# Performance work log

Hardware: AMD Instinct MI355X
Metric: run time of the kernel (lower is better)

## Reference

```python
import jax, jax.numpy as jnp
import numpy as np

DECAY = 0.6
THRESH = 0.6
MASK_T = 784 * 4  # default T in create_general_mask


def _make_mask(dim, c_min=10, c_max=50, min_dc=0.95, max_dc=0.99, T=MASK_T):
    # Faithful numpy port of create_general_mask (phase_shift_max=0.0 -> no shift).
    dcs = np.linspace(min_dc, max_dc, dim)
    cycles = np.linspace(c_min, c_max, dim)
    rows = []
    for cyc, dc in zip(cycles, dcs):
        cyc = int(np.ceil(cyc))
        on = int(np.ceil(dc * cyc))
        pat = [1] * on + [0] * (cyc - on)
        full = pat * (T // cyc) + pat[: T % cyc]
        rows.append(full)
    return jnp.asarray(np.array(rows, dtype=np.float32))  # [dim, T]


def setup_inputs() -> dict:
    key = jax.random.key(0)
    k1, k2, k3, k4, k5 = jax.random.split(key, 5)
    T, B, NTOKEN, NINP, H1, H2 = 128, 32, 32000, 256, 512, 512
    raw_input = jax.random.randint(k1, (T, B), 0, NTOKEN)
    enc_w = jax.random.uniform(k2, (NTOKEN, NINP), jnp.float32, -0.1, 0.1)
    # kaiming_uniform-like init: bound = sqrt(6 / fan_in), torch fan_in = dim 1
    b1 = float(np.sqrt(6.0 / H1))
    b2 = float(np.sqrt(6.0 / H2))
    fc1 = jax.random.uniform(k3, (NINP, H1), jnp.float32, -b1, b1)
    fc2 = jax.random.uniform(k4, (H1, H2), jnp.float32, -b2, b2)
    dec_w = jax.random.uniform(k5, (NTOKEN, H2), jnp.float32, -0.1, 0.1)
    dec_b = jnp.zeros((NTOKEN,), jnp.float32)
    mask1 = _make_mask(H1)
    mask2 = _make_mask(H2)
    return {"raw_input": raw_input, "enc_w": enc_w, "fc1": fc1, "fc2": fc2,
            "dec_w": dec_w, "dec_b": dec_b, "mask1": mask1, "mask2": mask2}


def _act(x):
    # ActFun.forward: heaviside spike
    return (x > 0.0).astype(x.dtype)


def reference(raw_input, enc_w, fc1, fc2, dec_w, dec_b, mask1, mask2):
    T, B = raw_input.shape
    emb = enc_w[raw_input]                    # [T, B, ninp] (dropout p=0 -> identity)
    m1 = mask1[:, :T].T                       # [T, H1]
    m2 = mask2[:, :T].T                       # [T, H2]

    def rhythm_update(fc, x, mem, m):
        state = x @ fc                        # [B, H]
        reset = (mem > THRESH).astype(x.dtype)
        new_mem = mem * (1.0 - reset) * DECAY + state
        mem = jnp.where(m == 0.0, mem, new_mem)   # mask broadcasts [H] -> [B, H]
        spike = _act(mem - THRESH) * m
        return mem, spike

    h1 = jnp.zeros((B, fc1.shape[1]), emb.dtype)
    h2 = jnp.zeros((B, fc2.shape[1]), emb.dtype)

    def step(carry, xs):
        h1m, h2m = carry
        x, ma, mb = xs
        h1m, s1 = rhythm_update(fc1, x, h1m, ma)
        h2m, s2 = rhythm_update(fc2, s1, h2m, mb)
        return (h1m, h2m), s2

    _, spikes = jax.lax.scan(step, (h1, h2), (emb, m1, m2))  # [T, B, H2]
    decoded = spikes @ dec_w.T + dec_b        # [T, B, ntoken]
    return decoded
```

## Files before the change

### kernel.cpp

```cpp
#include <hip/hip_runtime.h>


typedef __attribute__((ext_vector_type(8))) short short8;
typedef __attribute__((ext_vector_type(4))) float f32x4;
typedef __attribute__((ext_vector_type(8))) unsigned short us8;

#define WAITVM(N) asm volatile("s_waitcnt vmcnt(" #N ")" ::: "memory")
#define LGKM0()   asm volatile("s_waitcnt lgkmcnt(0)" ::: "memory")

__device__ __forceinline__ unsigned short f2bf(float f) {
    unsigned int u = __float_as_uint(f);
    unsigned int r = (u + 0x7FFFu + ((u >> 16) & 1u)) >> 16;
    return (unsigned short)r;
}

__global__ __launch_bounds__(256) void maskT_kernel(
    const float* __restrict__ m1, const float* __restrict__ m2,
    float* __restrict__ t1, float* __restrict__ t2)
{
    int i = blockIdx.x * 256 + threadIdx.x;
    int h = i >> 7, t = i & 127;
    t1[t * 512 + h] = m1[(size_t)h * 3136 + t];
    t2[t * 512 + h] = m2[(size_t)h * 3136 + t];
}

__global__ __launch_bounds__(256) void split_kernel(
    const float* __restrict__ w, unsigned short* __restrict__ w2, int n4)
{
    int i = blockIdx.x * 256 + threadIdx.x;
    if (i >= n4) return;
    float4 v = ((const float4*)w)[i];
    float vv[4] = {v.x, v.y, v.z, v.w};
    us8 o;
    #pragma unroll
    for (int c = 0; c < 4; ++c) {
        unsigned short hb = f2bf(vv[c]);
        float hf = __uint_as_float(((unsigned int)hb) << 16);
        o[2 * c]     = hb;
        o[2 * c + 1] = f2bf(vv[c] - hf);
    }
    ((us8*)w2)[i] = o;
}

__global__ __launch_bounds__(256) void gemm_f32_kernel(
    const float* __restrict__ A, const float* __restrict__ B,
    float* __restrict__ C, int M, int N, int K,
    const int* __restrict__ gidx, const float* __restrict__ gtable)
{
    __shared__ float As[16][64];
    __shared__ float Bs[16][64];
    int tid = threadIdx.x;
    int bn0 = blockIdx.x * 64, bm0 = blockIdx.y * 64;

    int lrowA = tid >> 2;
    int lkA   = (tid & 3) * 4;
    int lkB   = tid >> 4;
    int lnB   = (tid & 15) * 4;
    int ty = tid >> 4, tx = tid & 15;

    const float* Abase;
    size_t aoff;
    int grow = bm0 + lrowA;
    if (gidx) { Abase = gtable; aoff = (size_t)gidx[grow] * K; }
    else      { Abase = A;      aoff = (size_t)grow * K; }

    float acc[4][4];
    #pragma unroll
    for (int i = 0; i < 4; ++i)
        #pragma unroll
        for (int j = 0; j < 4; ++j) acc[i][j] = 0.f;

    for (int k0 = 0; k0 < K; k0 += 16) {
        float4 av = *(const float4*)(Abase + aoff + k0 + lkA);
        As[lkA + 0][lrowA] = av.x;
        As[lkA + 1][lrowA] = av.y;
        As[lkA + 2][lrowA] = av.z;
        As[lkA + 3][lrowA] = av.w;
        float4 bv = *(const float4*)(B + (size_t)(k0 + lkB) * N + bn0 + lnB);
        *(float4*)&Bs[lkB][lnB] = bv;
        __syncthreads();
        #pragma unroll
        for (int kk = 0; kk < 16; ++kk) {
            float4 aq = *(float4*)&As[kk][ty * 4];
            float4 bq = *(float4*)&Bs[kk][tx * 4];
            float aa[4] = {aq.x, aq.y, aq.z, aq.w};
            float bb[4] = {bq.x, bq.y, bq.z, bq.w};
            #pragma unroll
            for (int i = 0; i < 4; ++i)
                #pragma unroll
                for (int j = 0; j < 4; ++j) acc[i][j] += aa[i] * bb[j];
        }
        __syncthreads();
    }
    #pragma unroll
    for (int i = 0; i < 4; ++i) {
        float4 v = {acc[i][0], acc[i][1], acc[i][2], acc[i][3]};
        *(float4*)(C + (size_t)(bm0 + ty * 4 + i) * N + bn0 + tx * 4) = v;
    }
}

template <int DUP>
__global__ __launch_bounds__(64) void scan_kernel(
    const float* __restrict__ state, const float* __restrict__ maskT,
    float* __restrict__ outF, unsigned int* __restrict__ outU)
{
    int tid = blockIdx.x * 64 + threadIdx.x;
    int b = tid >> 9, h = tid & 511;
    float mem = 0.f;
    for (int t0 = 0; t0 < 128; t0 += 8) {
        float st8[8], m8[8];
        #pragma unroll
        for (int u = 0; u < 8; ++u) {
            st8[u] = state[(size_t)((t0 + u) * 32 + b) * 512 + h];
            m8[u]  = maskT[(t0 + u) * 512 + h];
        }
        #pragma unroll
        for (int u = 0; u < 8; ++u) {
            float nm = (mem > 0.6f) ? st8[u] : mem * 0.6f + st8[u];
            mem = (m8[u] == 0.0f) ? mem : nm;
            float spf = (mem > 0.6f) ? m8[u] : 0.0f;
            size_t ridx = (size_t)((t0 + u) * 32 + b) * 512 + h;
            if (DUP) outU[ridx] = f2bf(spf) * 0x10001u;
            else     outF[ridx] = spf;
        }
    }
}

__global__ __launch_bounds__(512, 2) void gemm3_kernel(
    const unsigned short* __restrict__ A,
    const unsigned short* __restrict__ W,
    const float* __restrict__ bias, float* __restrict__ C)
{
    constexpr int K = 1024, NTOK = 32000;
    __shared__ char lds[131072];

    int tid  = threadIdx.x;
    int lane = tid & 63;
    int wid  = __builtin_amdgcn_readfirstlane(tid >> 6);

    int bid = blockIdx.x;
    int swz = (bid & 7) * 250 + (bid >> 3);
    int mt = swz & 15;
    int nt = swz >> 4;
    int m0 = mt * 256, n0 = nt * 256;

    int wm = wid >> 2, wn = wid & 3;

    const unsigned short* srcB[4];
    int dstOff[4];
    #pragma unroll
    for (int i = 0; i < 4; ++i) {
        int q   = i * 512 + tid;
        int isB = q >> 10;
        int qq  = q & 1023;
        int j   = qq >> 3;
        int cp  = qq & 7;
        int c   = cp ^ (j & 7);
        int row = 2 * j + (c >> 2);
        srcB[i] = (isB ? W + (size_t)(n0 + row) * K
                       : A + (size_t)(m0 + row) * K) + (c & 3) * 8;
        dstOff[i] = (i * 512 + wid * 64) * 16;
    }

    int r = lane & 15, co = lane >> 4;
    int aOff[8], bOff[4];
    #pragma unroll
    for (int mf = 0; mf < 8; ++mf) {
        int row = wm * 128 + mf * 16 + r;
        int j = row >> 1, c = co + 4 * (row & 1);
        aOff[mf] = (j * 8 + (c ^ (j & 7))) * 16;
    }
    #pragma unroll
    for (int nf = 0; nf < 4; ++nf) {
        int row = wn * 64 + nf * 16 + r;
        int j = row >> 1, c = co + 4 * (row & 1);
        bOff[nf] = 16384 + (j * 8 + (c ^ (j & 7))) * 16;
    }

    f32x4 acc[8][4];
    #pragma unroll
    for (int i = 0; i < 8; ++i)
        #pragma unroll
        for (int j = 0; j < 4; ++j) acc[i][j] = (f32x4){0.f, 0.f, 0.f, 0.f};

    auto GLOAD = [&](int i, int kt) {
        __builtin_amdgcn_global_load_lds(
            (const __attribute__((address_space(1))) unsigned int*)(srcB[i] + kt * 32),
            (__attribute__((address_space(3))) unsigned int*)(lds + ((kt & 3) << 15) + dstOff[i]),
            16, 0, 0);
    };

    auto STEP = [&](int t, bool stage) {
        const char* base = lds + ((t & 3) << 15);
        short8 fa0[4], fb[4], fa1[4];
        if (stage) { GLOAD(0, t + 3); GLOAD(1, t + 3); }
        #pragma unroll
        for (int f = 0; f < 4; ++f) fa0[f] = *(const short8*)(base + aOff[f]);
        #pragma unroll
        for (int f = 0; f < 4; ++f) fb[f]  = *(const short8*)(base + bOff[f]);
        __builtin_amdgcn_s_barrier();
        LGKM0();
        __builtin_amdgcn_s_setprio(1);
        #pragma unroll
        for (int mf = 0; mf < 4; ++mf)
            #pragma unroll
            for (int nf = 0; nf < 4; ++nf)
                acc[mf][nf] = __builtin_amdgcn_mfma_f32_16x16x32_bf16(
                    fa0[mf], fb[nf], acc[mf][nf], 0, 0, 0);
        __builtin_amdgcn_s_setprio(0);
        __builtin_amdgcn_s_barrier();
        if (stage) { GLOAD(2, t + 3); GLOAD(3, t + 3); }
        #pragma unroll
        for (int f = 0; f < 4; ++f) fa1[f] = *(const short8*)(base + aOff[4 + f]);
        __builtin_amdgcn_s_barrier();
        LGKM0();
        __builtin_amdgcn_s_setprio(1);
        #pragma unroll
        for (int mf = 0; mf < 4; ++mf)
            #pragma unroll
            for (int nf = 0; nf < 4; ++nf)
                acc[4 + mf][nf] = __builtin_amdgcn_mfma_f32_16x16x32_bf16(
                    fa1[mf], fb[nf], acc[4 + mf][nf], 0, 0, 0);
        __builtin_amdgcn_s_setprio(0);
    };

    #pragma unroll
    for (int kt = 0; kt < 3; ++kt)
        #pragma unroll
        for (int i = 0; i < 4; ++i) GLOAD(i, kt);
    WAITVM(8);
    __builtin_amdgcn_s_barrier();

    for (int t = 0; t < 29; ++t) {
        STEP(t, true);
        WAITVM(8);
        __builtin_amdgcn_s_barrier();
    }
    STEP(29, false);
    WAITVM(4);
    __builtin_amdgcn_s_barrier();
    STEP(30, false);
    WAITVM(0);
    __builtin_amdgcn_s_barrier();
    STEP(31, false);

    int lr = lane >> 4, lc = lane & 15;
    #pragma unroll
    for (int nf = 0; nf < 4; ++nf) {
        int gc = n0 + wn * 64 + nf * 16 + lc;
        float bv = bias[gc];
        #pragma unroll
        for (int mf = 0; mf < 8; ++mf) {
            int gr = m0 + wm * 128 + mf * 16 + lr * 4;
            f32x4 v = acc[mf][nf];
            #pragma unroll
            for (int j = 0; j < 4; ++j)
                C[(size_t)(gr + j) * NTOK + gc] = v[j] + bv;
        }
    }
}

extern "C" void kernel_launch(void* const* d_in, const int* in_sizes, int n_in,
                              void* d_out, int out_size, void* d_ws, size_t ws_size,
                              hipStream_t stream)
{
    const int*   raw   = (const int*)  d_in[0];
    const float* enc_w = (const float*)d_in[1];
    const float* fc1   = (const float*)d_in[2];
    const float* fc2   = (const float*)d_in[3];
    const float* dec_w = (const float*)d_in[4];
    const float* dec_b = (const float*)d_in[5];
    const float* mask1 = (const float*)d_in[6];
    const float* mask2 = (const float*)d_in[7];
    float* out = (float*)d_out;

    const int H1 = 512, H2 = 512, NINP = 256, NTOK = 32000;
    const int M = 128 * 32;

    char* ws = (char*)d_ws;
    float*          st  = (float*)ws;
    float*          spF = (float*)(ws + (size_t)(8u << 20));
    unsigned int*   a2u = (unsigned int*)(ws + (size_t)(8u << 20));
    unsigned short* A2  = (unsigned short*)(ws + (size_t)(8u << 20));
    unsigned short* W2  = (unsigned short*)(ws + (size_t)(16u << 20));
    float* mT1 = (float*)d_out;
    float* mT2 = (float*)d_out + 65536;

    maskT_kernel<<<256, 256, 0, stream>>>(mask1, mask2, mT1, mT2);

    int n4 = NTOK * H2 / 4;
    split_kernel<<<(n4 + 255) / 256, 256, 0, stream>>>(dec_w, W2, n4);

    gemm_f32_kernel<<<dim3(H1 / 64, M / 64), 256, 0, stream>>>(
        nullptr, fc1, st, M, H1, NINP, raw, enc_w);

    scan_kernel<0><<<256, 64, 0, stream>>>(st, mT1, spF, nullptr);

    gemm_f32_kernel<<<dim3(H2 / 64, M / 64), 256, 0, stream>>>(
        spF, fc2, st, M, H2, H1, nullptr, nullptr);

    scan_kernel<1><<<256, 64, 0, stream>>>(st, mT2, nullptr, a2u);

    gemm3_kernel<<<(M / 256) * (NTOK / 256), 512, 0, stream>>>(A2, W2, dec_b, out);

    (void)in_sizes; (void)n_in; (void)out_size; (void)ws_size;
}
```

Before: 932.5 us.

## Switch decoder GEMM to 32x32x16 MFMA and enlarge fp32 GEMM tiles

The decoder GEMM moves from 16x16x32 bf16 MFMA fragments to 32x32x16 fragments. The LDS fragment offsets, the per-k-half loads and the epilogue row mapping are rewritten to match, so fewer, larger MFMAs and fewer LDS reads are issued per step. Separately, the fp32 GEMMs for fc1 and fc2 now use a 128x64 tile with K=32 per stage, padded LDS, and global loads issued before the barrier, which halves the grid. The cost is more registers per thread in the fp32 GEMM, more complex index mapping, and fewer blocks for small GEMMs.

```diff
diff --git a/kernel.cpp b/kernel.cpp
--- a/kernel.cpp
+++ b/kernel.cpp
@@ -1,9 +1,9 @@
 #include <hip/hip_runtime.h>
 
 
-typedef __attribute__((ext_vector_type(8))) short short8;
-typedef __attribute__((ext_vector_type(4))) float f32x4;
-typedef __attribute__((ext_vector_type(8))) unsigned short us8;
+typedef __attribute__((ext_vector_type(8)))  short short8;
+typedef __attribute__((ext_vector_type(16))) float f32x16;
+typedef __attribute__((ext_vector_type(8)))  unsigned short us8;
 
 #define WAITVM(N) asm volatile("s_waitcnt vmcnt(" #N ")" ::: "memory")
 #define LGKM0()   asm volatile("s_waitcnt lgkmcnt(0)" ::: "memory")
@@ -47,55 +47,70 @@
     float* __restrict__ C, int M, int N, int K,
     const int* __restrict__ gidx, const float* __restrict__ gtable)
 {
-    __shared__ float As[16][64];
-    __shared__ float Bs[16][64];
+    __shared__ float As[32][132];
+    __shared__ float Bs[32][68];
     int tid = threadIdx.x;
-    int bn0 = blockIdx.x * 64, bm0 = blockIdx.y * 64;
-
-    int lrowA = tid >> 2;
-    int lkA   = (tid & 3) * 4;
-    int lkB   = tid >> 4;
-    int lnB   = (tid & 15) * 4;
+    int bn0 = blockIdx.x * 64, bm0 = blockIdx.y * 128;
     int ty = tid >> 4, tx = tid & 15;
 
+    int arL  = tid >> 1;
+    int akh  = (tid & 1) * 16;
     const float* Abase;
     size_t aoff;
-    int grow = bm0 + lrowA;
-    if (gidx) { Abase = gtable; aoff = (size_t)gidx[grow] * K; }
-    else      { Abase = A;      aoff = (size_t)grow * K; }
-
-    float acc[4][4];
-    #pragma unroll
-    for (int i = 0; i < 4; ++i)
+    {
+        int grow = bm0 + arL;
+        if (gidx) { Abase = gtable; aoff = (size_t)gidx[grow] * K; }
+        else      { Abase = A;      aoff = (size_t)grow * K; }
+    }
+
+    float acc[8][4];
+    #pragma unroll
+    for (int i = 0; i < 8; ++i)
         #pragma unroll
         for (int j = 0; j < 4; ++j) acc[i][j] = 0.f;
 
-    for (int k0 = 0; k0 < K; k0 += 16) {
-        float4 av = *(const float4*)(Abase + aoff + k0 + lkA);
-        As[lkA + 0][lrowA] = av.x;
-        As[lkA + 1][lrowA] = av.y;
-        As[lkA + 2][lrowA] = av.z;
-        As[lkA + 3][lrowA] = av.w;
-        float4 bv = *(const float4*)(B + (size_t)(k0 + lkB) * N + bn0 + lnB);
-        *(float4*)&Bs[lkB][lnB] = bv;
+    for (int k0 = 0; k0 < K; k0 += 32) {
+        float4 a4[4];
+        #pragma unroll
+        for (int i = 0; i < 4; ++i)
+            a4[i] = *(const float4*)(Abase + aoff + k0 + akh + i * 4);
+        float4 b4[2];
+        #pragma unroll
+        for (int i = 0; i < 2; ++i) {
+            int f = tid + 256 * i;
+            b4[i] = *(const float4*)(B + (size_t)(k0 + (f >> 4)) * N + bn0 + (f & 15) * 4);
+        }
         __syncthreads();
         #pragma unroll
-        for (int kk = 0; kk < 16; ++kk) {
-            float4 aq = *(float4*)&As[kk][ty * 4];
-            float4 bq = *(float4*)&Bs[kk][tx * 4];
-            float aa[4] = {aq.x, aq.y, aq.z, aq.w};
+        for (int i = 0; i < 4; ++i) {
+            As[akh + i * 4 + 0][arL] = a4[i].x;
+            As[akh + i * 4 + 1][arL] = a4[i].y;
+            As[akh + i * 4 + 2][arL] = a4[i].z;
+            As[akh + i * 4 + 3][arL] = a4[i].w;
+        }
+        #pragma unroll
+        for (int i = 0; i < 2; ++i) {
+            int f = tid + 256 * i;
+            *(float4*)&Bs[f >> 4][(f & 15) * 4] = b4[i];
+        }
+        __syncthreads();
+        #pragma unroll
+        for (int kk = 0; kk < 32; ++kk) {
+            float a8[8];
+            *(float4*)&a8[0] = *(const float4*)&As[kk][ty * 8];
+            *(float4*)&a8[4] = *(const float4*)&As[kk][ty * 8 + 4];
+            float4 bq = *(const float4*)&Bs[kk][tx * 4];
             float bb[4] = {bq.x, bq.y, bq.z, bq.w};
             #pragma unroll
-            for (int i = 0; i < 4; ++i)
+            for (int i = 0; i < 8; ++i)
                 #pragma unroll
-                for (int j = 0; j < 4; ++j) acc[i][j] += aa[i] * bb[j];
-        }
-        __syncthreads();
-    }
-    #pragma unroll
-    for (int i = 0; i < 4; ++i) {
+                for (int j = 0; j < 4; ++j) acc[i][j] += a8[i] * bb[j];
+        }
+    }
+    #pragma unroll
+    for (int i = 0; i < 8; ++i) {
         float4 v = {acc[i][0], acc[i][1], acc[i][2], acc[i][3]};
-        *(float4*)(C + (size_t)(bm0 + ty * 4 + i) * N + bn0 + tx * 4) = v;
+        *(float4*)(C + (size_t)(bm0 + ty * 8 + i) * N + bn0 + tx * 4) = v;
     }
 }
 
@@ -162,26 +177,30 @@
         dstOff[i] = (i * 512 + wid * 64) * 16;
     }
 
-    int r = lane & 15, co = lane >> 4;
-    int aOff[8], bOff[4];
-    #pragma unroll
-    for (int mf = 0; mf < 8; ++mf) {
-        int row = wm * 128 + mf * 16 + r;
-        int j = row >> 1, c = co + 4 * (row & 1);
-        aOff[mf] = (j * 8 + (c ^ (j & 7))) * 16;
-    }
-    #pragma unroll
-    for (int nf = 0; nf < 4; ++nf) {
-        int row = wn * 64 + nf * 16 + r;
-        int j = row >> 1, c = co + 4 * (row & 1);
-        bOff[nf] = 16384 + (j * 8 + (c ^ (j & 7))) * 16;
-    }
-
-    f32x4 acc[8][4];
-    #pragma unroll
-    for (int i = 0; i < 8; ++i)
-        #pragma unroll
-        for (int j = 0; j < 4; ++j) acc[i][j] = (f32x4){0.f, 0.f, 0.f, 0.f};
+    int cl = lane & 31, hi5 = lane >> 5;
+    int aOff[4], bOff[2];
+    #pragma unroll
+    for (int mi = 0; mi < 4; ++mi) {
+        int R = wm * 128 + mi * 32 + cl;
+        int j = R >> 1;
+        int c = (hi5 + 4 * (R & 1)) ^ (j & 7);
+        aOff[mi] = j * 128 + c * 16;
+    }
+    #pragma unroll
+    for (int ni = 0; ni < 2; ++ni) {
+        int R = wn * 64 + ni * 32 + cl;
+        int j = R >> 1;
+        int c = (hi5 + 4 * (R & 1)) ^ (j & 7);
+        bOff[ni] = 16384 + j * 128 + c * 16;
+    }
+
+    f32x16 acc[4][2];
+    #pragma unroll
+    for (int i = 0; i < 4; ++i)
+        #pragma unroll
+        for (int j = 0; j < 2; ++j)
+            #pragma unroll
+            for (int e = 0; e < 16; ++e) acc[i][j][e] = 0.f;
 
     auto GLOAD = [&](int i, int kt) {
         __builtin_amdgcn_global_load_lds(
@@ -192,36 +211,29 @@
 
     auto STEP = [&](int t, bool stage) {
         const char* base = lds + ((t & 3) << 15);
-        short8 fa0[4], fb[4], fa1[4];
-        if (stage) { GLOAD(0, t + 3); GLOAD(1, t + 3); }
-        #pragma unroll
-        for (int f = 0; f < 4; ++f) fa0[f] = *(const short8*)(base + aOff[f]);
-        #pragma unroll
-        for (int f = 0; f < 4; ++f) fb[f]  = *(const short8*)(base + bOff[f]);
-        __builtin_amdgcn_s_barrier();
-        LGKM0();
-        __builtin_amdgcn_s_setprio(1);
-        #pragma unroll
-        for (int mf = 0; mf < 4; ++mf)
-            #pragma unroll
-            for (int nf = 0; nf < 4; ++nf)
-                acc[mf][nf] = __builtin_amdgcn_mfma_f32_16x16x32_bf16(
-                    fa0[mf], fb[nf], acc[mf][nf], 0, 0, 0);
-        __builtin_amdgcn_s_setprio(0);
-        __builtin_amdgcn_s_barrier();
-        if (stage) { GLOAD(2, t + 3); GLOAD(3, t + 3); }
-        #pragma unroll
-        for (int f = 0; f < 4; ++f) fa1[f] = *(const short8*)(base + aOff[4 + f]);
-        __builtin_amdgcn_s_barrier();
-        LGKM0();
-        __builtin_amdgcn_s_setprio(1);
-        #pragma unroll
-        for (int mf = 0; mf < 4; ++mf)
-            #pragma unroll
-            for (int nf = 0; nf < 4; ++nf)
-                acc[4 + mf][nf] = __builtin_amdgcn_mfma_f32_16x16x32_bf16(
-                    fa1[mf], fb[nf], acc[4 + mf][nf], 0, 0, 0);
-        __builtin_amdgcn_s_setprio(0);
+        #pragma unroll
+        for (int ki = 0; ki < 2; ++ki) {
+            if (stage) { GLOAD(2 * ki, t + 3); GLOAD(2 * ki + 1, t + 3); }
+            short8 fa[4], fb[2];
+            int kx = ki * 32;
+            #pragma unroll
+            for (int mi = 0; mi < 4; ++mi)
+                fa[mi] = *(const short8*)(base + (aOff[mi] ^ kx));
+            #pragma unroll
+            for (int ni = 0; ni < 2; ++ni)
+                fb[ni] = *(const short8*)(base + (bOff[ni] ^ kx));
+            __builtin_amdgcn_s_barrier();
+            LGKM0();
+            __builtin_amdgcn_sched_barrier(0);
+            __builtin_amdgcn_s_setprio(1);
+            #pragma unroll
+            for (int mi = 0; mi < 4; ++mi)
+                #pragma unroll
+                for (int ni = 0; ni < 2; ++ni)
+                    acc[mi][ni] = __builtin_amdgcn_mfma_f32_32x32x16_bf16(
+                        fa[mi], fb[ni], acc[mi][ni], 0, 0, 0);
+            __builtin_amdgcn_s_setprio(0);
+        }
     };
 
     #pragma unroll
@@ -244,18 +256,18 @@
     __builtin_amdgcn_s_barrier();
     STEP(31, false);
 
-    int lr = lane >> 4, lc = lane & 15;
-    #pragma unroll
-    for (int nf = 0; nf < 4; ++nf) {
-        int gc = n0 + wn * 64 + nf * 16 + lc;
+    #pragma unroll
+    for (int ni = 0; ni < 2; ++ni) {
+        int gc = n0 + wn * 64 + ni * 32 + cl;
         float bv = bias[gc];
         #pragma unroll
-        for (int mf = 0; mf < 8; ++mf) {
-            int gr = m0 + wm * 128 + mf * 16 + lr * 4;
-            f32x4 v = acc[mf][nf];
-            #pragma unroll
-            for (int j = 0; j < 4; ++j)
-                C[(size_t)(gr + j) * NTOK + gc] = v[j] + bv;
+        for (int mi = 0; mi < 4; ++mi) {
+            f32x16 v = acc[mi][ni];
+            #pragma unroll
+            for (int reg = 0; reg < 16; ++reg) {
+                int gr = m0 + wm * 128 + mi * 32 + (reg & 3) + 8 * (reg >> 2) + 4 * hi5;
+                C[(size_t)gr * NTOK + gc] = v[reg] + bv;
+            }
         }
     }
 }
@@ -291,12 +303,12 @@
     int n4 = NTOK * H2 / 4;
     split_kernel<<<(n4 + 255) / 256, 256, 0, stream>>>(dec_w, W2, n4);
 
-    gemm_f32_kernel<<<dim3(H1 / 64, M / 64), 256, 0, stream>>>(
+    gemm_f32_kernel<<<dim3(H1 / 64, M / 128), 256, 0, stream>>>(
         nullptr, fc1, st, M, H1, NINP, raw, enc_w);
 
     scan_kernel<0><<<256, 64, 0, stream>>>(st, mT1, spF, nullptr);
 
-    gemm_f32_kernel<<<dim3(H2 / 64, M / 64), 256, 0, stream>>>(
+    gemm_f32_kernel<<<dim3(H2 / 64, M / 128), 256, 0, stream>>>(
         spF, fc2, st, M, H2, H1, nullptr, nullptr);
 
     scan_kernel<1><<<256, 64, 0, stream>>>(st, mT2, nullptr, a2u);
```

Measured after the change: 916.1 us. No clear change (-1.8%).
